# Kernel optimization log

Hardware: AMD Instinct MI355X
Metric: run time of the kernel (lower is better)

The kernel has to match this reference:

```python
import jax, jax.numpy as jnp
import numpy as np

# Megablocks block-sparse MoE FFN (SwiGLU), modeled as a grouped GEMM over
# experts with tokens pre-sorted into equal-size per-expert groups.
E = 8        # num experts
T = 1024     # tokens per expert
D = 2048     # in_features (d_model)
H = 4096     # per-expert FFN hidden (hidden_features = E*H = 32768)
W_STD = 0.02


def setup_inputs() -> dict:
    key = jax.random.key(0)
    k_x, k1, k2, k3 = jax.random.split(key, 4)
    x = jax.random.normal(k_x, (E * T, D), dtype=jnp.float32)
    # Stacked expert weights, each [hidden_features, in_features] like the torch module.
    w1 = jax.random.normal(k1, (E * H, D), dtype=jnp.float32) * W_STD
    w2 = jax.random.normal(k2, (E * H, D), dtype=jnp.float32) * W_STD
    w3 = jax.random.normal(k3, (E * H, D), dtype=jnp.float32) * W_STD
    return {"x": x, "w1": w1, "w2": w2, "w3": w3, "num_experts": E}


def reference(x, w1, w2, w3, num_experts):
    n_tok, d = x.shape
    t_per_e = n_tok // num_experts
    xg = x.reshape(num_experts, t_per_e, d)            # [E, T, D] tokens grouped by expert
    w1g = w1.reshape(num_experts, -1, d)               # [E, H, D]
    w2g = w2.reshape(num_experts, -1, d)
    w3g = w3.reshape(num_experts, -1, d)
    # sdd_nt: per-expert x @ w^T -> block-sparse activation [E, T, H]
    h1 = jnp.einsum('etd,ehd->eth', xg, w1g)
    h3 = jnp.einsum('etd,ehd->eth', xg, w3g)
    gated = jax.nn.silu(h1) * h3                        # SwiGLU act_fn
    # dsd_nn: per-expert act @ w2 -> dense output [E, T, D]
    out = jnp.einsum('eth,ehd->etd', gated, w2g)
    return out.reshape(n_tok, d)
```

## Files before the change

kernel.cpp:

```cpp
#include <hip/hip_runtime.h>
#include <hip/hip_bf16.h>

#define NE 8
#define NT 1024
#define ND 2048
#define NH 4096

typedef __attribute__((ext_vector_type(8))) short bf16x8;
typedef __attribute__((ext_vector_type(4))) float f32x4;

#define ASYNC_COPY16(g, l) __builtin_amdgcn_global_load_lds( \
    (const __attribute__((address_space(1))) void*)(g),      \
    (__attribute__((address_space(3))) void*)(l), 16, 0, 0)

__global__ __launch_bounds__(256) void convert_bf16_kernel(
    const float* __restrict__ src, __hip_bfloat16* __restrict__ dst, int n4)
{
  const int stride = gridDim.x * 256;
  for (int i = blockIdx.x * 256 + threadIdx.x; i < n4; i += stride) {
    const float4 v = reinterpret_cast<const float4*>(src)[i];
    union { ushort4 u; __hip_bfloat16 h[4]; } o;
    o.h[0] = __float2bfloat16(v.x);
    o.h[1] = __float2bfloat16(v.y);
    o.h[2] = __float2bfloat16(v.z);
    o.h[3] = __float2bfloat16(v.w);
    reinterpret_cast<ushort4*>(dst)[i] = o.u;
  }
}

__global__ __launch_bounds__(256) void transpose_bf16_kernel(
    const float* __restrict__ src, __hip_bfloat16* __restrict__ dst)
{
  __shared__ float tile[32][33];
  const int e  = blockIdx.z;
  const int d0 = blockIdx.x * 32, h0 = blockIdx.y * 32;
  const int tx = threadIdx.x, ty = threadIdx.y;
  const float* s = src + (size_t)e * NH * ND;
  __hip_bfloat16* t = dst + (size_t)e * ND * NH;
#pragma unroll
  for (int i = 0; i < 32; i += 8)
    tile[ty + i][tx] = s[(size_t)(h0 + ty + i) * ND + d0 + tx];
  __syncthreads();
#pragma unroll
  for (int i = 0; i < 32; i += 8)
    t[(size_t)(d0 + ty + i) * NH + h0 + tx] = __float2bfloat16(tile[tx][ty + i]);
}

__global__ __launch_bounds__(256, 2) void stage1_kernel(
    const __hip_bfloat16* __restrict__ xb,
    const __hip_bfloat16* __restrict__ w1b,
    const __hip_bfloat16* __restrict__ w3b,
    __hip_bfloat16* __restrict__ gated)
{
  constexpr int BM = 128, BN = 128, BK = 32;
  __shared__ __hip_bfloat16 lA [BM * BK];
  __shared__ __hip_bfloat16 lB1[BN * BK];
  __shared__ __hip_bfloat16 lB3[BN * BK];

  const int tid  = threadIdx.x;
  const int wave = tid >> 6, lane = tid & 63;

  constexpr int tilesM = NT / BM;
  const int bid = blockIdx.x;
  const int e      = bid & 7;
  const int within = bid >> 3;
  const int tn = within >> 3;
  const int tm = within & (tilesM - 1);

  const __hip_bfloat16* Ab  = xb  + ((size_t)e * NT + (size_t)tm * BM) * ND;
  const __hip_bfloat16* B1b = w1b + ((size_t)e * NH + (size_t)tn * BN) * ND;
  const __hip_bfloat16* B3b = w3b + ((size_t)e * NH + (size_t)tn * BN) * ND;

  const int rowL = lane >> 2;
  const int colL = (lane & 3) * 8;
  const int wr = wave >> 1, wc = wave & 1;
  const int fRow = lane & 15, fK = (lane >> 4) * 8;

  f32x4 acc1[4][4] = {};
  f32x4 acc3[4][4] = {};

  for (int k0 = 0; k0 < ND; k0 += BK) {
#pragma unroll
    for (int i = 0; i < 2; ++i) {
      const int c = wave + i * 4;
      const int row = c * 16 + rowL;
      ASYNC_COPY16(Ab  + (size_t)row * ND + k0 + colL, (char*)lA  + c * 1024);
      ASYNC_COPY16(B1b + (size_t)row * ND + k0 + colL, (char*)lB1 + c * 1024);
      ASYNC_COPY16(B3b + (size_t)row * ND + k0 + colL, (char*)lB3 + c * 1024);
    }
    __syncthreads();

    bf16x8 fA[4], fB1[4], fB3[4];
#pragma unroll
    for (int q = 0; q < 4; ++q) {
      fA[q]  = *(const bf16x8*)&lA [(wr * 64 + q * 16 + fRow) * BK + fK];
      fB1[q] = *(const bf16x8*)&lB1[(wc * 64 + q * 16 + fRow) * BK + fK];
      fB3[q] = *(const bf16x8*)&lB3[(wc * 64 + q * 16 + fRow) * BK + fK];
    }
#pragma unroll
    for (int im = 0; im < 4; ++im)
#pragma unroll
      for (int in = 0; in < 4; ++in) {
        acc1[im][in] = __builtin_amdgcn_mfma_f32_16x16x32_bf16(fA[im], fB1[in], acc1[im][in], 0, 0, 0);
        acc3[im][in] = __builtin_amdgcn_mfma_f32_16x16x32_bf16(fA[im], fB3[in], acc3[im][in], 0, 0, 0);
      }
    __syncthreads();
  }

  __hip_bfloat16* g = gated + (size_t)e * NT * NH;
  const int or0 = tm * BM + wr * 64;
  const int oc0 = tn * BN + wc * 64;
#pragma unroll
  for (int im = 0; im < 4; ++im)
#pragma unroll
    for (int in = 0; in < 4; ++in)
#pragma unroll
      for (int r = 0; r < 4; ++r) {
        const int row = or0 + im * 16 + (lane >> 4) * 4 + r;
        const int col = oc0 + in * 16 + (lane & 15);
        const float h1 = acc1[im][in][r];
        const float h3 = acc3[im][in][r];
        const float sw = h1 / (1.f + __expf(-h1)) * h3;
        g[(size_t)row * NH + col] = __float2bfloat16(sw);
      }
}

__global__ __launch_bounds__(256, 2) void stage2_kernel(
    const __hip_bfloat16* __restrict__ gated,
    const __hip_bfloat16* __restrict__ w2t,
    float* __restrict__ out)
{
  constexpr int BM = 128, BN = 128, BK = 32;
  __shared__ __hip_bfloat16 lA[BM * BK];
  __shared__ __hip_bfloat16 lB[BN * BK];

  const int tid  = threadIdx.x;
  const int wave = tid >> 6, lane = tid & 63;

  constexpr int tilesM = NT / BM;
  const int bid = blockIdx.x;
  const int e      = bid & 7;
  const int within = bid >> 3;
  const int tn = within >> 3;
  const int tm = within & (tilesM - 1);

  const __hip_bfloat16* Ab = gated + (size_t)e * NT * NH + (size_t)tm * BM * NH;
  const __hip_bfloat16* Bb = w2t   + (size_t)e * ND * NH + (size_t)tn * BN * NH;

  const int rowL = lane >> 2, colL = (lane & 3) * 8;
  const int wr = wave >> 1, wc = wave & 1;
  const int fRow = lane & 15, fK = (lane >> 4) * 8;

  f32x4 acc[4][4] = {};

  for (int k0 = 0; k0 < NH; k0 += BK) {
#pragma unroll
    for (int i = 0; i < 2; ++i) {
      const int c = wave + i * 4;
      const int row = c * 16 + rowL;
      ASYNC_COPY16(Ab + (size_t)row * NH + k0 + colL, (char*)lA + c * 1024);
      ASYNC_COPY16(Bb + (size_t)row * NH + k0 + colL, (char*)lB + c * 1024);
    }
    __syncthreads();

    bf16x8 fA[4], fB[4];
#pragma unroll
    for (int q = 0; q < 4; ++q) {
      fA[q] = *(const bf16x8*)&lA[(wr * 64 + q * 16 + fRow) * BK + fK];
      fB[q] = *(const bf16x8*)&lB[(wc * 64 + q * 16 + fRow) * BK + fK];
    }
#pragma unroll
    for (int im = 0; im < 4; ++im)
#pragma unroll
      for (int in = 0; in < 4; ++in)
        acc[im][in] = __builtin_amdgcn_mfma_f32_16x16x32_bf16(fA[im], fB[in], acc[im][in], 0, 0, 0);
    __syncthreads();
  }

  const int or0 = tm * BM + wr * 64;
  const int oc0 = tn * BN + wc * 64;
  float* obase = out + (size_t)e * NT * ND;
#pragma unroll
  for (int im = 0; im < 4; ++im)
#pragma unroll
    for (int in = 0; in < 4; ++in)
#pragma unroll
      for (int r = 0; r < 4; ++r) {
        const int row = or0 + im * 16 + (lane >> 4) * 4 + r;
        const int col = oc0 + in * 16 + (lane & 15);
        obase[(size_t)row * ND + col] = acc[im][in][r];
      }
}

extern "C" void kernel_launch(void* const* d_in, const int* in_sizes, int n_in,
                              void* d_out, int out_size, void* d_ws, size_t ws_size,
                              hipStream_t stream) {
  const float* x  = (const float*)d_in[0];
  const float* w1 = (const float*)d_in[1];
  const float* w2 = (const float*)d_in[2];
  const float* w3 = (const float*)d_in[3];
  float* out = (float*)d_out;

  char* ws = (char*)d_ws;
  const size_t MB = 1ull << 20;
  __hip_bfloat16* xb    = (__hip_bfloat16*)(ws);
  __hip_bfloat16* w1b   = (__hip_bfloat16*)(ws + 32 * MB);
  __hip_bfloat16* w3b   = (__hip_bfloat16*)(ws + 160 * MB);
  __hip_bfloat16* w2t   = (__hip_bfloat16*)(ws + 288 * MB);
  __hip_bfloat16* gated = (__hip_bfloat16*)(ws + 416 * MB);

  const int nx = NE * NT * ND;
  const int nw = NE * NH * ND;

  convert_bf16_kernel<<<2048, 256, 0, stream>>>(x,  xb,  nx / 4);
  convert_bf16_kernel<<<2048, 256, 0, stream>>>(w1, w1b, nw / 4);
  convert_bf16_kernel<<<2048, 256, 0, stream>>>(w3, w3b, nw / 4);
  transpose_bf16_kernel<<<dim3(ND / 32, NH / 32, NE), dim3(32, 8), 0, stream>>>(w2, w2t);

  stage1_kernel<<<NE * (NT / 128) * (NH / 128), 256, 0, stream>>>(xb, w1b, w3b, gated);
  stage2_kernel<<<NE * (NT / 128) * (ND / 128), 256, 0, stream>>>(gated, w2t, out);
}
```

Before: 1.312 ms.

## Double K tile to 64 and XOR-swizzle LDS layout in both GEMM stages

```diff
diff --git a/kernel.cpp b/kernel.cpp
--- a/kernel.cpp
+++ b/kernel.cpp
@@ -46,13 +46,19 @@
     t[(size_t)(d0 + ty + i) * NH + h0 + tx] = __float2bfloat16(tile[tx][ty + i]);
 }
 
+__device__ __forceinline__ bf16x8 lds_frag(const __hip_bfloat16* base, int row, int colElem)
+{
+  const char* p = (const char*)base + row * 128 + ((colElem << 1) ^ ((row & 7) << 4));
+  return *(const bf16x8*)p;
+}
+
 __global__ __launch_bounds__(256, 2) void stage1_kernel(
     const __hip_bfloat16* __restrict__ xb,
     const __hip_bfloat16* __restrict__ w1b,
     const __hip_bfloat16* __restrict__ w3b,
     __hip_bfloat16* __restrict__ gated)
 {
-  constexpr int BM = 128, BN = 128, BK = 32;
+  constexpr int BM = 128, BN = 128, BK = 64;
   __shared__ __hip_bfloat16 lA [BM * BK];
   __shared__ __hip_bfloat16 lB1[BN * BK];
   __shared__ __hip_bfloat16 lB3[BN * BK];
@@ -71,8 +77,8 @@
   const __hip_bfloat16* B1b = w1b + ((size_t)e * NH + (size_t)tn * BN) * ND;
   const __hip_bfloat16* B3b = w3b + ((size_t)e * NH + (size_t)tn * BN) * ND;
 
-  const int rowL = lane >> 2;
-  const int colL = (lane & 3) * 8;
+  const int srow = lane >> 3;
+  const int scol = ((lane & 7) ^ (lane >> 3)) << 3;
   const int wr = wave >> 1, wc = wave & 1;
   const int fRow = lane & 15, fK = (lane >> 4) * 8;
 
@@ -81,29 +87,33 @@
 
   for (int k0 = 0; k0 < ND; k0 += BK) {
 #pragma unroll
-    for (int i = 0; i < 2; ++i) {
-      const int c = wave + i * 4;
-      const int row = c * 16 + rowL;
-      ASYNC_COPY16(Ab  + (size_t)row * ND + k0 + colL, (char*)lA  + c * 1024);
-      ASYNC_COPY16(B1b + (size_t)row * ND + k0 + colL, (char*)lB1 + c * 1024);
-      ASYNC_COPY16(B3b + (size_t)row * ND + k0 + colL, (char*)lB3 + c * 1024);
-    }
-    __syncthreads();
-
-    bf16x8 fA[4], fB1[4], fB3[4];
-#pragma unroll
-    for (int q = 0; q < 4; ++q) {
-      fA[q]  = *(const bf16x8*)&lA [(wr * 64 + q * 16 + fRow) * BK + fK];
-      fB1[q] = *(const bf16x8*)&lB1[(wc * 64 + q * 16 + fRow) * BK + fK];
-      fB3[q] = *(const bf16x8*)&lB3[(wc * 64 + q * 16 + fRow) * BK + fK];
-    }
-#pragma unroll
-    for (int im = 0; im < 4; ++im)
-#pragma unroll
-      for (int in = 0; in < 4; ++in) {
-        acc1[im][in] = __builtin_amdgcn_mfma_f32_16x16x32_bf16(fA[im], fB1[in], acc1[im][in], 0, 0, 0);
-        acc3[im][in] = __builtin_amdgcn_mfma_f32_16x16x32_bf16(fA[im], fB3[in], acc3[im][in], 0, 0, 0);
-      }
+    for (int p = 0; p < 4; ++p) {
+      const int c = wave + p * 4;
+      const int row = c * 8 + srow;
+      const size_t go = (size_t)row * ND + k0 + scol;
+      ASYNC_COPY16(Ab  + go, (char*)lA  + c * 1024);
+      ASYNC_COPY16(B1b + go, (char*)lB1 + c * 1024);
+      ASYNC_COPY16(B3b + go, (char*)lB3 + c * 1024);
+    }
+    __syncthreads();
+
+#pragma unroll
+    for (int kk = 0; kk < 2; ++kk) {
+      bf16x8 fA[4], fB1[4], fB3[4];
+#pragma unroll
+      for (int q = 0; q < 4; ++q) {
+        fA[q]  = lds_frag(lA,  wr * 64 + q * 16 + fRow, kk * 32 + fK);
+        fB1[q] = lds_frag(lB1, wc * 64 + q * 16 + fRow, kk * 32 + fK);
+        fB3[q] = lds_frag(lB3, wc * 64 + q * 16 + fRow, kk * 32 + fK);
+      }
+#pragma unroll
+      for (int im = 0; im < 4; ++im)
+#pragma unroll
+        for (int in = 0; in < 4; ++in) {
+          acc1[im][in] = __builtin_amdgcn_mfma_f32_16x16x32_bf16(fA[im], fB1[in], acc1[im][in], 0, 0, 0);
+          acc3[im][in] = __builtin_amdgcn_mfma_f32_16x16x32_bf16(fA[im], fB3[in], acc3[im][in], 0, 0, 0);
+        }
+    }
     __syncthreads();
   }
 
@@ -130,7 +140,7 @@
     const __hip_bfloat16* __restrict__ w2t,
     float* __restrict__ out)
 {
-  constexpr int BM = 128, BN = 128, BK = 32;
+  constexpr int BM = 128, BN = 128, BK = 64;
   __shared__ __hip_bfloat16 lA[BM * BK];
   __shared__ __hip_bfloat16 lB[BN * BK];
 
@@ -147,7 +157,8 @@
   const __hip_bfloat16* Ab = gated + (size_t)e * NT * NH + (size_t)tm * BM * NH;
   const __hip_bfloat16* Bb = w2t   + (size_t)e * ND * NH + (size_t)tn * BN * NH;
 
-  const int rowL = lane >> 2, colL = (lane & 3) * 8;
+  const int srow = lane >> 3;
+  const int scol = ((lane & 7) ^ (lane >> 3)) << 3;
   const int wr = wave >> 1, wc = wave & 1;
   const int fRow = lane & 15, fK = (lane >> 4) * 8;
 
@@ -155,25 +166,29 @@
 
   for (int k0 = 0; k0 < NH; k0 += BK) {
 #pragma unroll
-    for (int i = 0; i < 2; ++i) {
-      const int c = wave + i * 4;
-      const int row = c * 16 + rowL;
-      ASYNC_COPY16(Ab + (size_t)row * NH + k0 + colL, (char*)lA + c * 1024);
-      ASYNC_COPY16(Bb + (size_t)row * NH + k0 + colL, (char*)lB + c * 1024);
-    }
-    __syncthreads();
-
-    bf16x8 fA[4], fB[4];
-#pragma unroll
-    for (int q = 0; q < 4; ++q) {
-      fA[q] = *(const bf16x8*)&lA[(wr * 64 + q * 16 + fRow) * BK + fK];
-      fB[q] = *(const bf16x8*)&lB[(wc * 64 + q * 16 + fRow) * BK + fK];
-    }
-#pragma unroll
-    for (int im = 0; im < 4; ++im)
-#pragma unroll
-      for (int in = 0; in < 4; ++in)
-        acc[im][in] = __builtin_amdgcn_mfma_f32_16x16x32_bf16(fA[im], fB[in], acc[im][in], 0, 0, 0);
+    for (int p = 0; p < 4; ++p) {
+      const int c = wave + p * 4;
+      const int row = c * 8 + srow;
+      const size_t go = (size_t)row * NH + k0 + scol;
+      ASYNC_COPY16(Ab + go, (char*)lA + c * 1024);
+      ASYNC_COPY16(Bb + go, (char*)lB + c * 1024);
+    }
+    __syncthreads();
+
+#pragma unroll
+    for (int kk = 0; kk < 2; ++kk) {
+      bf16x8 fA[4], fB[4];
+#pragma unroll
+      for (int q = 0; q < 4; ++q) {
+        fA[q] = lds_frag(lA, wr * 64 + q * 16 + fRow, kk * 32 + fK);
+        fB[q] = lds_frag(lB, wc * 64 + q * 16 + fRow, kk * 32 + fK);
+      }
+#pragma unroll
+      for (int im = 0; im < 4; ++im)
+#pragma unroll
+        for (int in = 0; in < 4; ++in)
+          acc[im][in] = __builtin_amdgcn_mfma_f32_16x16x32_bf16(fA[im], fB[in], acc[im][in], 0, 0, 0);
+    }
     __syncthreads();
   }
 
```

New measurement: 1.228 ms. -6.4%, faster.
